# Performance work log

Hardware: AMD Instinct MI355X
Metric: run time of the kernel (lower is better)

Reference implementation:

```python
import jax, jax.numpy as jnp
import numpy as np
from jax import lax

H = 192; W = 192; C = 256; N = H * W; E = 294912; K = 289; DSIG = 1
SLOPE = 0.01
EPS = 1e-5


def leaky(x):
    return jnp.where(x >= 0, x, SLOPE * x)


def conv2d(x, w, pad, groups):
    return lax.conv_general_dilated(
        x, w, (1, 1), [(pad, pad), (pad, pad)],
        dimension_numbers=('NCHW', 'OIHW', 'NCHW'),
        feature_group_count=groups)


def bn2d(x, g, b):
    # BatchNorm2d with track_running_stats=False -> always batch stats (biased var)
    m = x.mean(axis=(0, 2, 3), keepdims=True)
    v = x.var(axis=(0, 2, 3), keepdims=True)
    return (x - m) / jnp.sqrt(v + EPS) * g.reshape(1, -1, 1, 1) + b.reshape(1, -1, 1, 1)


def conv_batch(x, w, g, b, pad, groups):
    # nn.Sequential(LeakyReLU(0.01), Conv2d(bias=False), BatchNorm2d)
    return bn2d(conv2d(leaky(x), w, pad, groups), g, b)


def bn1d(x, g, b):
    m = x.mean(axis=0)
    v = x.var(axis=0)
    return (x - m) / jnp.sqrt(v + EPS) * g + b


def setup_inputs() -> dict:
    key = jax.random.key(0)
    ks = jax.random.split(key, 20)
    X = jax.random.normal(ks[0], (N, C), dtype=jnp.float32)
    src = jax.random.randint(ks[1], (E,), 0, N)
    dst = jax.random.randint(ks[2], (E,), 0, N)
    k1 = jax.random.randint(ks[3], (E,), 0, K)
    k2 = jax.random.randint(ks[4], (E,), 0, K)
    InfoIdx = jnp.stack([src, k1, dst, k2], axis=1).astype(jnp.int64)
    edgmsk = (jax.random.uniform(ks[5], (E, 1)) < 0.9).astype(jnp.float32)
    s = 0.05
    inp = {
        'X': X, 'InfoIdx': InfoIdx, 'edgmsk': edgmsk,
        # PPM: depthwise 17x17 conv_batch then 1x1 conv_batch
        'ppm_w0': jax.random.normal(ks[6], (C, 1, 17, 17), jnp.float32) * s,
        'ppm_g0': jnp.ones((C,), jnp.float32), 'ppm_b0': jnp.zeros((C,), jnp.float32),
        'ppm_w1': jax.random.normal(ks[7], (C, C, 1, 1), jnp.float32) * s,
        'ppm_g1': jnp.ones((C,), jnp.float32), 'ppm_b1': jnp.zeros((C,), jnp.float32),
        # FFN_1: two 1x1 conv_batch
        'ffn1_w0': jax.random.normal(ks[8], (C, C, 1, 1), jnp.float32) * s,
        'ffn1_g0': jnp.ones((C,), jnp.float32), 'ffn1_b0': jnp.zeros((C,), jnp.float32),
        'ffn1_w1': jax.random.normal(ks[9], (C, C, 1, 1), jnp.float32) * s,
        'ffn1_g1': jnp.ones((C,), jnp.float32), 'ffn1_b1': jnp.zeros((C,), jnp.float32),
        # Dis: Linear(C,C) -> LeakyReLU -> Linear(C, 289)
        'dis_w1': jax.random.normal(ks[10], (C, C), jnp.float32) * s,
        'dis_b1': jnp.zeros((C,), jnp.float32),
        'dis_w2': jax.random.normal(ks[11], (K * DSIG, C), jnp.float32) * s,
        'dis_b2': jnp.zeros((K * DSIG,), jnp.float32),
        # BatchNorm1d
        'bn_g': jnp.ones((C,), jnp.float32), 'bn_b': jnp.zeros((C,), jnp.float32),
        # FFN_2 = DoubleConv: depthwise-expand 3x3 (groups=C, out=4C) then 1x1
        'ffn2_w0': jax.random.normal(ks[12], (4 * C, 1, 3, 3), jnp.float32) * s,
        'ffn2_g0': jnp.ones((4 * C,), jnp.float32), 'ffn2_b0': jnp.zeros((4 * C,), jnp.float32),
        'ffn2_w1': jax.random.normal(ks[13], (C, 4 * C, 1, 1), jnp.float32) * s,
        'ffn2_g1': jnp.ones((C,), jnp.float32), 'ffn2_b1': jnp.zeros((C,), jnp.float32),
    }
    return inp


def reference(X, InfoIdx, edgmsk,
              ppm_w0, ppm_g0, ppm_b0, ppm_w1, ppm_g1, ppm_b1,
              ffn1_w0, ffn1_g0, ffn1_b0, ffn1_w1, ffn1_g1, ffn1_b1,
              dis_w1, dis_b1, dis_w2, dis_b2, bn_g, bn_b,
              ffn2_w0, ffn2_g0, ffn2_b0, ffn2_w1, ffn2_g1, ffn2_b1):
    src_idx = InfoIdx[:, 0]
    dst_idx = InfoIdx[:, 2]
    # [N,C] -> [1,C,H,W]
    img = X.T.reshape(1, C, H, W)
    # PPM residual
    t = conv_batch(img, ppm_w0, ppm_g0, ppm_b0, pad=8, groups=C)
    t = conv_batch(t, ppm_w1, ppm_g1, ppm_b1, pad=0, groups=1)
    img = img + t
    # FFN_1 residual
    t = conv_batch(img, ffn1_w0, ffn1_g0, ffn1_b0, pad=0, groups=1)
    t = conv_batch(t, ffn1_w1, ffn1_g1, ffn1_b1, pad=0, groups=1)
    img = img + t
    Xn = img.reshape(C, N).T  # [N, C]
    # Dis MLP -> signal [N, 289, d_signal]
    h = leaky(Xn @ dis_w1.T + dis_b1)
    signal = (h @ dis_w2.T + dis_b2).reshape(N, K, DSIG)
    # edge gather + exp/clamp score
    s_src = signal[src_idx, InfoIdx[:, 1]]  # [E, 1]
    s_dst = signal[dst_idx, InfoIdx[:, 3]]  # [E, 1]
    aij = jnp.exp(jnp.clip(s_src + s_dst, -5.0, 5.0)) * edgmsk  # [E, 1]
    # two scatter-sum reductions to dst nodes
    A_sum = jax.ops.segment_sum(aij, dst_idx, num_segments=N)  # [N, 1]
    XA_sum = jax.ops.segment_sum(Xn[src_idx] * aij, dst_idx, num_segments=N)  # [N, C]
    X_trans = XA_sum / (A_sum + 1e-5)
    Xn = Xn + bn1d(X_trans, bn_g, bn_b)
    # FFN_2 = DoubleConv with residual skip
    img = Xn.T.reshape(1, C, H, W)
    t = conv_batch(img, ffn2_w0, ffn2_g0, ffn2_b0, pad=1, groups=C)
    t = conv_batch(t, ffn2_w1, ffn2_g1, ffn2_b1, pad=0, groups=1)
    out = t + img
    return out.reshape(C, N).T  # final bg.ndata['X'], [N, C]
```

## Files before the change

### kernel.cpp

```cpp
#include <hip/hip_runtime.h>
#include <cstddef>

#define HW 192
#define NP 36864
#define CH 256
#define EDGES 294912
#define KSIG 289
#define SLOPE 0.01f
#define BNEPS 1e-5f

typedef unsigned short u16;
typedef __attribute__((ext_vector_type(8))) short bf16x8;
typedef __attribute__((ext_vector_type(4))) float f32x4;

__device__ __forceinline__ float leaky(float x) { return x >= 0.f ? x : SLOPE * x; }
__device__ __forceinline__ u16 f2bf(float x) {
  unsigned u = __float_as_uint(x);
  unsigned r = (u + 0x7fffu + ((u >> 16) & 1u)) >> 16;
  return (u16)r;
}
__device__ __forceinline__ float bf2f(unsigned h) { return __uint_as_float(h << 16); }
__device__ __forceinline__ void bnss(const float* sums, const float* sqs,
                                     const float* g, const float* b, int k,
                                     float& s, float& h) {
  float mean = sums[k] * (1.f / NP);
  float var = sqs[k] * (1.f / NP) - mean * mean;
  s = g[k] * rsqrtf(var + BNEPS);
  h = b[k] - mean * s;
}

__global__ __launch_bounds__(256) void k_transpose(const float* __restrict__ src,
                                                   float* __restrict__ dst, int R, int S) {
  __shared__ float tile[32][33];
  int s0 = blockIdx.x * 32, r0 = blockIdx.y * 32;
  int tx = threadIdx.x & 31, ty = threadIdx.x >> 5;
#pragma unroll
  for (int j = 0; j < 4; j++) {
    int r = r0 + ty + 8 * j;
    tile[ty + 8 * j][tx] = src[(size_t)r * S + s0 + tx];
  }
  __syncthreads();
#pragma unroll
  for (int j = 0; j < 4; j++) {
    int s = s0 + ty + 8 * j;
    dst[(size_t)s * R + r0 + tx] = tile[tx][ty + 8 * j];
  }
}

__global__ __launch_bounds__(256) void k_cvtW(const float* __restrict__ pw1,
                                              const float* __restrict__ f1w0,
                                              const float* __restrict__ f1w1,
                                              const float* __restrict__ dw1,
                                              const float* __restrict__ dw2,
                                              const float* __restrict__ f2w1,
                                              u16* __restrict__ out) {
  int i = blockIdx.x * 256 + threadIdx.x;
  float v;
  if (i < 65536) v = pw1[i];
  else if (i < 131072) v = f1w0[i - 65536];
  else if (i < 196608) v = f1w1[i - 131072];
  else if (i < 262144) v = dw1[i - 196608];
  else if (i < 360448) { int j = i - 262144; v = (j < KSIG * 256) ? dw2[j] : 0.f; }
  else v = f2w1[i - 360448];
  out[i] = f2bf(v);
}

__global__ __launch_bounds__(256) void k_stats_f32(const float* __restrict__ Xr,
                                                   float* __restrict__ sums,
                                                   float* __restrict__ sqs) {
  int row = blockIdx.x;
  int t = threadIdx.x;
  const float4* p = (const float4*)(Xr + (size_t)row * NP);
  float s = 0.f, q = 0.f;
  for (int i = t; i < NP / 4; i += 256) {
    float4 v = p[i];
    s += v.x + v.y + v.z + v.w;
    q += v.x * v.x + v.y * v.y + v.z * v.z + v.w * v.w;
  }
  __shared__ float ss[256], qq[256];
  ss[t] = s; qq[t] = q;
  __syncthreads();
  for (int d = 128; d > 0; d >>= 1) {
    if (t < d) { ss[t] += ss[t + d]; qq[t] += qq[t + d]; }
    __syncthreads();
  }
  if (t == 0) { sums[row] = ss[0]; sqs[row] = qq[0]; }
}

__global__ __launch_bounds__(256) void k_stats_bf(const u16* __restrict__ Xr,
                                                  float* __restrict__ sums,
                                                  float* __restrict__ sqs) {
  int row = blockIdx.x;
  int t = threadIdx.x;
  const uint4* p = (const uint4*)(Xr + (size_t)row * NP);
  float s = 0.f, q = 0.f;
  for (int i = t; i < NP / 8; i += 256) {
    uint4 v = p[i];
    unsigned w[4] = {v.x, v.y, v.z, v.w};
#pragma unroll
    for (int j = 0; j < 4; j++) {
      float a = bf2f(w[j] & 0xffffu), c = bf2f(w[j] >> 16);
      s += a + c; q += a * a + c * c;
    }
  }
  __shared__ float ss[256], qq[256];
  ss[t] = s; qq[t] = q;
  __syncthreads();
  for (int d = 128; d > 0; d >>= 1) {
    if (t < d) { ss[t] += ss[t + d]; qq[t] += qq[t + d]; }
    __syncthreads();
  }
  if (t == 0) { sums[row] = ss[0]; sqs[row] = qq[0]; }
}

__global__ __launch_bounds__(256) void k_cvtT(const float* __restrict__ in,
                                              u16* __restrict__ outT, int M) {
  __shared__ float tile[32][65];
  int n0 = blockIdx.x * 64, k0 = blockIdx.y * 32;
  int t = threadIdx.x;
#pragma unroll
  for (int i = 0; i < 2; i++) {
    int ci = i * 256 + t;
    int k = ci >> 4, cg = (ci & 15) * 4;
    float4 v = *(const float4*)&in[(size_t)(k0 + k) * NP + n0 + cg];
    tile[k][cg] = v.x; tile[k][cg + 1] = v.y; tile[k][cg + 2] = v.z; tile[k][cg + 3] = v.w;
  }
  __syncthreads();
  int n = t >> 2, kg = (t & 3) * 8;
  uint4 o;
  o.x = (unsigned)f2bf(tile[kg + 0][n]) | ((unsigned)f2bf(tile[kg + 1][n]) << 16);
  o.y = (unsigned)f2bf(tile[kg + 2][n]) | ((unsigned)f2bf(tile[kg + 3][n]) << 16);
  o.z = (unsigned)f2bf(tile[kg + 4][n]) | ((unsigned)f2bf(tile[kg + 5][n]) << 16);
  o.w = (unsigned)f2bf(tile[kg + 6][n]) | ((unsigned)f2bf(tile[kg + 7][n]) << 16);
  *(uint4*)&outT[(size_t)(n0 + n) * M + k0 + kg] = o;
}

__global__ __launch_bounds__(256) void k_cvtTs(const float* __restrict__ in,
                                               u16* __restrict__ outT,
                                               const float* __restrict__ sums,
                                               const float* __restrict__ sqs,
                                               const float* __restrict__ g,
                                               const float* __restrict__ b, int M) {
  __shared__ float tile[32][65];
  int n0 = blockIdx.x * 64, k0 = blockIdx.y * 32;
  int t = threadIdx.x;
#pragma unroll
  for (int i = 0; i < 2; i++) {
    int ci = i * 256 + t;
    int k = ci >> 4, cg = (ci & 15) * 4;
    float s, h; bnss(sums, sqs, g, b, k0 + k, s, h);
    float4 v = *(const float4*)&in[(size_t)(k0 + k) * NP + n0 + cg];
    tile[k][cg]     = leaky(fmaf(v.x, s, h));
    tile[k][cg + 1] = leaky(fmaf(v.y, s, h));
    tile[k][cg + 2] = leaky(fmaf(v.z, s, h));
    tile[k][cg + 3] = leaky(fmaf(v.w, s, h));
  }
  __syncthreads();
  int n = t >> 2, kg = (t & 3) * 8;
  uint4 o;
  o.x = (unsigned)f2bf(tile[kg + 0][n]) | ((unsigned)f2bf(tile[kg + 1][n]) << 16);
  o.y = (unsigned)f2bf(tile[kg + 2][n]) | ((unsigned)f2bf(tile[kg + 3][n]) << 16);
  o.z = (unsigned)f2bf(tile[kg + 4][n]) | ((unsigned)f2bf(tile[kg + 5][n]) << 16);
  o.w = (unsigned)f2bf(tile[kg + 6][n]) | ((unsigned)f2bf(tile[kg + 7][n]) << 16);
  *(uint4*)&outT[(size_t)(n0 + n) * M + k0 + kg] = o;
}

__global__ __launch_bounds__(256) void k_cvtT_bf(const u16* __restrict__ in,
                                                 u16* __restrict__ outT,
                                                 const float* __restrict__ sums,
                                                 const float* __restrict__ sqs,
                                                 const float* __restrict__ g,
                                                 const float* __restrict__ b, int M) {
  __shared__ float tile[32][65];
  int n0 = blockIdx.x * 64, k0 = blockIdx.y * 32;
  int t = threadIdx.x;
  int k = t >> 3, cg = (t & 7) * 8;
  float s, h; bnss(sums, sqs, g, b, k0 + k, s, h);
  uint4 v = *(const uint4*)&in[(size_t)(k0 + k) * NP + n0 + cg];
  unsigned w[4] = {v.x, v.y, v.z, v.w};
#pragma unroll
  for (int j = 0; j < 4; j++) {
    tile[k][cg + 2 * j]     = leaky(fmaf(bf2f(w[j] & 0xffffu), s, h));
    tile[k][cg + 2 * j + 1] = leaky(fmaf(bf2f(w[j] >> 16), s, h));
  }
  __syncthreads();
  int n = t >> 2, kg = (t & 3) * 8;
  uint4 o;
  o.x = (unsigned)f2bf(tile[kg + 0][n]) | ((unsigned)f2bf(tile[kg + 1][n]) << 16);
  o.y = (unsigned)f2bf(tile[kg + 2][n]) | ((unsigned)f2bf(tile[kg + 3][n]) << 16);
  o.z = (unsigned)f2bf(tile[kg + 4][n]) | ((unsigned)f2bf(tile[kg + 5][n]) << 16);
  o.w = (unsigned)f2bf(tile[kg + 6][n]) | ((unsigned)f2bf(tile[kg + 7][n]) << 16);
  *(uint4*)&outT[(size_t)(n0 + n) * M + k0 + kg] = o;
}

__global__ __launch_bounds__(256) void k_fuse1(const float* __restrict__ base,
                                               const float* __restrict__ raw,
                                               const float* __restrict__ sums,
                                               const float* __restrict__ sqs,
                                               const float* __restrict__ g,
                                               const float* __restrict__ b,
                                               float* __restrict__ img2,
                                               u16* __restrict__ outT) {
  __shared__ float tile[32][65];
  int n0 = blockIdx.x * 64, k0 = blockIdx.y * 32;
  int t = threadIdx.x;
#pragma unroll
  for (int i = 0; i < 2; i++) {
    int ci = i * 256 + t;
    int k = ci >> 4, cg = (ci & 15) * 4;
    float s, h; bnss(sums, sqs, g, b, k0 + k, s, h);
    size_t idx = (size_t)(k0 + k) * NP + n0 + cg;
    float4 bv = *(const float4*)&base[idx];
    float4 rv = *(const float4*)&raw[idx];
    float4 o;
    o.x = bv.x + fmaf(rv.x, s, h); o.y = bv.y + fmaf(rv.y, s, h);
    o.z = bv.z + fmaf(rv.z, s, h); o.w = bv.w + fmaf(rv.w, s, h);
    *(float4*)&img2[idx] = o;
    tile[k][cg]     = leaky(o.x);
    tile[k][cg + 1] = leaky(o.y);
    tile[k][cg + 2] = leaky(o.z);
    tile[k][cg + 3] = leaky(o.w);
  }
  __syncthreads();
  int n = t >> 2, kg = (t & 3) * 8;
  uint4 o;
  o.x = (unsigned)f2bf(tile[kg + 0][n]) | ((unsigned)f2bf(tile[kg + 1][n]) << 16);
  o.y = (unsigned)f2bf(tile[kg + 2][n]) | ((unsigned)f2bf(tile[kg + 3][n]) << 16);
  o.z = (unsigned)f2bf(tile[kg + 4][n]) | ((unsigned)f2bf(tile[kg + 5][n]) << 16);
  o.w = (unsigned)f2bf(tile[kg + 6][n]) | ((unsigned)f2bf(tile[kg + 7][n]) << 16);
  *(uint4*)&outT[(size_t)(n0 + n) * CH + k0 + kg] = o;
}

__global__ __launch_bounds__(256) void k_fuse2(const float* __restrict__ base,
                                               const float* __restrict__ raw,
                                               const float* __restrict__ sums,
                                               const float* __restrict__ sqs,
                                               const float* __restrict__ g,
                                               const float* __restrict__ b,
                                               float* __restrict__ XnT,
                                               u16* __restrict__ outT) {
  __shared__ float tile[32][65];
  int n0 = blockIdx.x * 64, k0 = blockIdx.y * 32;
  int t = threadIdx.x;
#pragma unroll
  for (int i = 0; i < 2; i++) {
    int ci = i * 256 + t;
    int k = ci >> 4, cg = (ci & 15) * 4;
    float s, h; bnss(sums, sqs, g, b, k0 + k, s, h);
    size_t idx = (size_t)(k0 + k) * NP + n0 + cg;
    float4 bv = *(const float4*)&base[idx];
    float4 rv = *(const float4*)&raw[idx];
    tile[k][cg]     = bv.x + fmaf(rv.x, s, h);
    tile[k][cg + 1] = bv.y + fmaf(rv.y, s, h);
    tile[k][cg + 2] = bv.z + fmaf(rv.z, s, h);
    tile[k][cg + 3] = bv.w + fmaf(rv.w, s, h);
  }
  __syncthreads();
  int n = t >> 2, kg = (t & 3) * 8;
  float4 f0 = {tile[kg + 0][n], tile[kg + 1][n], tile[kg + 2][n], tile[kg + 3][n]};
  float4 f1 = {tile[kg + 4][n], tile[kg + 5][n], tile[kg + 6][n], tile[kg + 7][n]};
  *(float4*)&XnT[(size_t)(n0 + n) * CH + k0 + kg] = f0;
  *(float4*)&XnT[(size_t)(n0 + n) * CH + k0 + kg + 4] = f1;
  uint4 o;
  o.x = (unsigned)f2bf(f0.x) | ((unsigned)f2bf(f0.y) << 16);
  o.y = (unsigned)f2bf(f0.z) | ((unsigned)f2bf(f0.w) << 16);
  o.z = (unsigned)f2bf(f1.x) | ((unsigned)f2bf(f1.y) << 16);
  o.w = (unsigned)f2bf(f1.z) | ((unsigned)f2bf(f1.w) << 16);
  *(uint4*)&outT[(size_t)(n0 + n) * CH + k0 + kg] = o;
}

__global__ __launch_bounds__(256) void k_mgemm(const u16* __restrict__ A,
                                               const u16* __restrict__ Bt,
                                               float* __restrict__ Out,
                                               const float* __restrict__ bias,
                                               int K, int Mstore, int actout) {
  __shared__ u16 As[128 * 32];
  __shared__ u16 Bs[128 * 32];
  int t = threadIdx.x;
  int lane = t & 63, wave = t >> 6;
  int wm = (wave >> 1) * 64, wn = (wave & 1) * 64;
  int m0 = blockIdx.y * 128, n0 = blockIdx.x * 128;
  int r = lane & 15, q = lane >> 4;
  f32x4 acc[4][4];
#pragma unroll
  for (int a = 0; a < 4; a++)
#pragma unroll
    for (int b = 0; b < 4; b++) acc[a][b] = (f32x4){0.f, 0.f, 0.f, 0.f};

  for (int k0 = 0; k0 < K; k0 += 32) {
#pragma unroll
    for (int i = 0; i < 2; i++) {
      int cc = t + i * 256;
      int mm = cc >> 2, kq = (cc & 3) * 8;
      uint4 av = *(const uint4*)&A[(size_t)(m0 + mm) * K + k0 + kq];
      uint4 bv = *(const uint4*)&Bt[(size_t)(n0 + mm) * K + k0 + kq];
      *(uint4*)&As[mm * 32 + kq] = av;
      *(uint4*)&Bs[mm * 32 + kq] = bv;
    }
    __syncthreads();
    bf16x8 af[4], bfr[4];
#pragma unroll
    for (int mt = 0; mt < 4; mt++)
      af[mt] = *(const bf16x8*)&As[(wm + mt * 16 + r) * 32 + q * 8];
#pragma unroll
    for (int nt = 0; nt < 4; nt++)
      bfr[nt] = *(const bf16x8*)&Bs[(wn + nt * 16 + r) * 32 + q * 8];
#pragma unroll
    for (int mt = 0; mt < 4; mt++)
#pragma unroll
      for (int nt = 0; nt < 4; nt++)
        acc[mt][nt] = __builtin_amdgcn_mfma_f32_16x16x32_bf16(af[mt], bfr[nt], acc[mt][nt], 0, 0, 0);
    __syncthreads();
  }
#pragma unroll
  for (int mt = 0; mt < 4; mt++) {
    int mrow = m0 + wm + mt * 16 + q * 4;
#pragma unroll
    for (int i = 0; i < 4; i++) {
      int m = mrow + i;
      if (m >= Mstore) continue;
      float bs = bias ? bias[m] : 0.f;
#pragma unroll
      for (int nt = 0; nt < 4; nt++) {
        float v = acc[mt][nt][i] + bs;
        if (actout) v = leaky(v);
        Out[(size_t)m * NP + n0 + wn + nt * 16 + r] = v;
      }
    }
  }
}

__global__ __launch_bounds__(256) void k_dwconv17(const float* __restrict__ in,
                                                  const float* __restrict__ w,
                                                  float* __restrict__ out) {
  int c = blockIdx.y;
  int tile = blockIdx.x;
  int ty0 = (tile / 3) * 64, tx0 = (tile % 3) * 64;
  __shared__ u16 smIn[80 * 88];
  __shared__ u16 smT[17 * 16 * 40];
  const float* inc = in + (size_t)c * NP;
  for (int i = threadIdx.x; i < 80 * 80; i += 256) {
    int r = i / 80, cc = i - r * 80;
    int gy = ty0 + r - 8, gx = tx0 + cc - 8;
    float v = 0.f;
    if (gy >= 0 && gy < HW && gx >= 0 && gx < HW) v = leaky(inc[gy * HW + gx]);
    smIn[r * 88 + cc] = f2bf(v);
  }
  const float* wc = w + c * 289;
  for (int i = threadIdx.x; i < 17 * 16 * 32; i += 256) {
    int ky = i >> 9;
    int rem = i & 511;
    int n = rem >> 5, kk = rem & 31;
    int kx = kk - n;
    float v = (kx >= 0 && kx < 17) ? wc[ky * 17 + kx] : 0.f;
    smT[(ky * 16 + n) * 40 + kk] = f2bf(v);
  }
  __syncthreads();
  int lane = threadIdx.x & 63, wave = threadIdx.x >> 6;
  int wy = wave * 16;
  int r = lane & 15, q = lane >> 4;
  f32x4 acc[4];
#pragma unroll
  for (int xt = 0; xt < 4; xt++) acc[xt] = (f32x4){0.f, 0.f, 0.f, 0.f};
#pragma unroll
  for (int ky = 0; ky < 17; ky++) {
    bf16x8 bfrag = *(const bf16x8*)&smT[(ky * 16 + r) * 40 + q * 8];
    int rowA = wy + r + ky;
#pragma unroll
    for (int xt = 0; xt < 4; xt++) {
      bf16x8 afrag = *(const bf16x8*)&smIn[rowA * 88 + xt * 16 + q * 8];
      acc[xt] = __builtin_amdgcn_mfma_f32_16x16x32_bf16(afrag, bfrag, acc[xt], 0, 0, 0);
    }
  }
  float* oc = out + (size_t)c * NP;
#pragma unroll
  for (int xt = 0; xt < 4; xt++) {
    int x = tx0 + xt * 16 + r;
#pragma unroll
    for (int i = 0; i < 4; i++) {
      int y = ty0 + wy + q * 4 + i;
      oc[y * HW + x] = acc[xt][i];
    }
  }
}

__global__ __launch_bounds__(256) void k_conv3x4(const float* __restrict__ in,
                                                 const float* __restrict__ w,
                                                 u16* __restrict__ out) {
  int wave = threadIdx.x >> 6, lane = threadIdx.x & 63;
  int c = blockIdx.y;
  int y = blockIdx.x * 4 + wave;
  const float* wc = w + (size_t)(4 * c) * 9;
  float wr[36];
#pragma unroll
  for (int k = 0; k < 36; k++) wr[k] = wc[k];
  float acc[4][3];
#pragma unroll
  for (int oc = 0; oc < 4; oc++)
#pragma unroll
    for (int s = 0; s < 3; s++) acc[oc][s] = 0.f;
  const float* base = in + (size_t)c * NP;
#pragma unroll
  for (int ky = 0; ky < 3; ky++) {
    int ry = y + ky - 1;
    if (ry < 0 || ry >= HW) continue;
    const float* rp = base + ry * HW;
    float a0 = leaky(rp[lane]);
    float a1 = leaky(rp[64 + lane]);
    float a2 = leaky(rp[128 + lane]);
    float e0 = __shfl(a0, 63), e1 = __shfl(a1, 63);
    float b1 = __shfl(a1, 0),  b2 = __shfl(a2, 0);
    float l0 = __shfl_up(a0, 1); if (lane == 0) l0 = 0.f;
    float l1 = __shfl_up(a1, 1); if (lane == 0) l1 = e0;
    float l2 = __shfl_up(a2, 1); if (lane == 0) l2 = e1;
    float r0 = __shfl_down(a0, 1); if (lane == 63) r0 = b1;
    float r1 = __shfl_down(a1, 1); if (lane == 63) r1 = b2;
    float r2 = __shfl_down(a2, 1); if (lane == 63) r2 = 0.f;
#pragma unroll
    for (int oc = 0; oc < 4; oc++) {
      float w0 = wr[oc * 9 + ky * 3], w1 = wr[oc * 9 + ky * 3 + 1], w2 = wr[oc * 9 + ky * 3 + 2];
      acc[oc][0] = fmaf(w0, l0, fmaf(w1, a0, fmaf(w2, r0, acc[oc][0])));
      acc[oc][1] = fmaf(w0, l1, fmaf(w1, a1, fmaf(w2, r1, acc[oc][1])));
      acc[oc][2] = fmaf(w0, l2, fmaf(w1, a2, fmaf(w2, r2, acc[oc][2])));
    }
  }
  size_t ob = (size_t)(4 * c) * NP + (size_t)y * HW + lane;
#pragma unroll
  for (int oc = 0; oc < 4; oc++) {
    out[ob + (size_t)oc * NP]       = f2bf(acc[oc][0]);
    out[ob + (size_t)oc * NP + 64]  = f2bf(acc[oc][1]);
    out[ob + (size_t)oc * NP + 128] = f2bf(acc[oc][2]);
  }
}

__global__ __launch_bounds__(256) void k_edge(const int* __restrict__ info,
                                              const float* __restrict__ msk,
                                              const float* __restrict__ sig,
                                              float* __restrict__ aij,
                                              int* __restrict__ counts) {
  int e = blockIdx.x * 256 + threadIdx.x;
  int4 ii = ((const int4*)info)[e];
  float s = sig[(size_t)ii.y * NP + ii.x] + sig[(size_t)ii.w * NP + ii.z];
  s = fminf(fmaxf(s, -5.f), 5.f);
  aij[e] = expf(s) * msk[e];
  atomicAdd(&counts[ii.z], 1);
}

__global__ __launch_bounds__(256) void k_scan1(const int* __restrict__ counts,
                                               int* __restrict__ offsets,
                                               int* __restrict__ bsum) {
  __shared__ int sm[256];
  int t = threadIdx.x;
  int i = blockIdx.x * 256 + t;
  int v = counts[i];
  sm[t] = v;
  __syncthreads();
  for (int d = 1; d < 256; d <<= 1) {
    int add = (t >= d) ? sm[t - d] : 0;
    __syncthreads();
    sm[t] += add;
    __syncthreads();
  }
  offsets[i] = sm[t] - v;
  if (t == 255) bsum[blockIdx.x] = sm[255];
}
__global__ __launch_bounds__(256) void k_scan2(const int* __restrict__ bsum,
                                               int* __restrict__ boff) {
  __shared__ int sm[256];
  int t = threadIdx.x;
  int v = (t < 144) ? bsum[t] : 0;
  sm[t] = v;
  __syncthreads();
  for (int d = 1; d < 256; d <<= 1) {
    int add = (t >= d) ? sm[t - d] : 0;
    __syncthreads();
    sm[t] += add;
    __syncthreads();
  }
  boff[t] = sm[t] - v;
}
__global__ __launch_bounds__(256) void k_scan3(int* __restrict__ offsets,
                                               const int* __restrict__ boff,
                                               int* __restrict__ cursor) {
  int i = blockIdx.x * 256 + threadIdx.x;
  int o = offsets[i] + boff[blockIdx.x];
  offsets[i] = o;
  cursor[i] = o;
  if (i == 0) offsets[NP] = EDGES;
}
__global__ __launch_bounds__(256) void k_scatter(const int* __restrict__ info,
                                                 int* __restrict__ cursor,
                                                 int* __restrict__ sorted) {
  int e = blockIdx.x * 256 + threadIdx.x;
  int d = info[4 * e + 2];
  int pos = atomicAdd(&cursor[d], 1);
  sorted[pos] = e;
}

__global__ __launch_bounds__(256) void k_agg(const int* __restrict__ offsets,
                                             const int* __restrict__ sorted,
                                             const float* __restrict__ aij,
                                             const int* __restrict__ info,
                                             const u16* __restrict__ XnBf,
                                             float* __restrict__ Xtr) {
  int wave = threadIdx.x >> 6, lane = threadIdx.x & 63;
  int node = blockIdx.x * 4 + wave;
  int o0 = offsets[node], o1 = offsets[node + 1];
  float ax = 0.f, ay = 0.f, az = 0.f, aw = 0.f, asum = 0.f;
  for (int i = o0; i < o1; i++) {
    int e = sorted[i];
    float a = aij[e];
    int s = info[4 * e];
    uint2 v = ((const uint2*)(XnBf + (size_t)s * CH))[lane];
    ax = fmaf(a, bf2f(v.x & 0xffffu), ax);
    ay = fmaf(a, bf2f(v.x >> 16), ay);
    az = fmaf(a, bf2f(v.y & 0xffffu), az);
    aw = fmaf(a, bf2f(v.y >> 16), aw);
    asum += a;
  }
  float inv = 1.f / (asum + 1e-5f);
  float4 o = {ax * inv, ay * inv, az * inv, aw * inv};
  ((float4*)(Xtr + (size_t)node * CH))[lane] = o;
}

__global__ __launch_bounds__(256) void k_colstats(const float* __restrict__ Xt,
                                                  float* __restrict__ sums,
                                                  float* __restrict__ sqs) {
  int c = threadIdx.x;
  float s = 0.f, q = 0.f;
  for (int n = blockIdx.x; n < NP; n += gridDim.x) {
    float v = Xt[(size_t)n * CH + c];
    s += v; q += v * v;
  }
  atomicAdd(&sums[c], s);
  atomicAdd(&sqs[c], q);
}

__global__ __launch_bounds__(256) void k_mkimg4(const float* __restrict__ Xn,
                                                const float* __restrict__ Xtr,
                                                const float* __restrict__ sums,
                                                const float* __restrict__ sqs,
                                                const float* __restrict__ g,
                                                const float* __restrict__ b,
                                                float* __restrict__ img4) {
  __shared__ float tile[32][33];
  int c0 = blockIdx.x * 32, n0 = blockIdx.y * 32;
  int tx = threadIdx.x & 31, ty = threadIdx.x >> 5;
  int c = c0 + tx;
  float s, h; bnss(sums, sqs, g, b, c, s, h);
#pragma unroll
  for (int j = 0; j < 4; j++) {
    size_t idx = (size_t)(n0 + ty + 8 * j) * CH + c;
    tile[ty + 8 * j][tx] = Xn[idx] + fmaf(Xtr[idx], s, h);
  }
  __syncthreads();
#pragma unroll
  for (int j = 0; j < 4; j++) {
    int cc = c0 + ty + 8 * j;
    img4[(size_t)cc * NP + n0 + tx] = tile[tx][ty + 8 * j];
  }
}

__global__ __launch_bounds__(256) void k_final(const float* __restrict__ raw5,
                                               const float* __restrict__ img4,
                                               const float* __restrict__ sums,
                                               const float* __restrict__ sqs,
                                               const float* __restrict__ g,
                                               const float* __restrict__ b,
                                               float* __restrict__ out) {
  __shared__ float tile[32][33];
  int n0 = blockIdx.x * 32, c0 = blockIdx.y * 32;
  int tx = threadIdx.x & 31, ty = threadIdx.x >> 5;
#pragma unroll
  for (int j = 0; j < 4; j++) {
    int c = c0 + ty + 8 * j;
    float s, h; bnss(sums, sqs, g, b, c, s, h);
    size_t idx = (size_t)c * NP + n0 + tx;
    tile[ty + 8 * j][tx] = fmaf(raw5[idx], s, h) + img4[idx];
  }
  __syncthreads();
#pragma unroll
  for (int j = 0; j < 4; j++) {
    int n = n0 + ty + 8 * j;
    out[(size_t)n * CH + c0 + tx] = tile[tx][ty + 8 * j];
  }
}

extern "C" void kernel_launch(void* const* d_in, const int* in_sizes, int n_in,
                              void* d_out, int out_size, void* d_ws, size_t ws_size,
                              hipStream_t stream) {
  (void)in_sizes; (void)n_in; (void)out_size; (void)ws_size;
  const float* X    = (const float*)d_in[0];
  const int*   info = (const int*)d_in[1];
  const float* msk  = (const float*)d_in[2];
  const float* pw0  = (const float*)d_in[3];
  const float* pg0  = (const float*)d_in[4];
  const float* pb0  = (const float*)d_in[5];
  const float* pw1  = (const float*)d_in[6];
  const float* pg1  = (const float*)d_in[7];
  const float* pb1  = (const float*)d_in[8];
  const float* f1w0 = (const float*)d_in[9];
  const float* f1g0 = (const float*)d_in[10];
  const float* f1b0 = (const float*)d_in[11];
  const float* f1w1 = (const float*)d_in[12];
  const float* f1g1 = (const float*)d_in[13];
  const float* f1b1 = (const float*)d_in[14];
  const float* dw1  = (const float*)d_in[15];
  const float* db1  = (const float*)d_in[16];
  const float* dw2  = (const float*)d_in[17];
  const float* db2  = (const float*)d_in[18];
  const float* bng  = (const float*)d_in[19];
  const float* bnb  = (const float*)d_in[20];
  const float* f2w0 = (const float*)d_in[21];
  const float* f2g0 = (const float*)d_in[22];
  const float* f2b0 = (const float*)d_in[23];
  const float* f2w1 = (const float*)d_in[24];
  const float* f2g1 = (const float*)d_in[25];
  const float* f2b1 = (const float*)d_in[26];
  float* out = (float*)d_out;

  float* ws = (float*)d_ws;
  float* sum0 = ws + 0;    float* sq0 = ws + 256;
  float* sum1 = ws + 512;  float* sq1 = ws + 768;
  float* sum2 = ws + 1024; float* sq2 = ws + 1280;
  float* sum3 = ws + 1536; float* sq3 = ws + 1792;
  float* sum5 = ws + 2048; float* sq5 = ws + 2304;
  float* sumT = ws + 2560; float* sqT = ws + 2816;
  float* sum4 = ws + 3072; float* sq4 = ws + 4096;
  int* counts  = (int*)(ws + 8192);
  int* offsets = (int*)(ws + 45056);
  int* cursor  = (int*)(ws + 82176);
  int* bsum    = (int*)(ws + 119296);
  int* boff    = (int*)(ws + 119552);
  int* sorted  = (int*)(ws + 131072);
  float* aij   = ws + 425984;
  const size_t S = (size_t)NP * CH;
  float* slotD = ws + 720896;
  float* slotB = slotD + S;
  float* slotA = slotB + S;
  float* slotC = slotA + S;
  u16* bfB  = (u16*)(slotC + S);
  u16* bfH  = bfB + S;
  float* sigT = (float*)(bfH + S);
  u16* bfW  = (u16*)(sigT + (size_t)KSIG * NP);
  u16* raw4bf  = (u16*)slotB;
  u16* bfT1024 = bfB;

  hipMemsetAsync(ws, 0, 5120 * sizeof(float), stream);
  hipMemsetAsync(counts, 0, NP * sizeof(int), stream);

  dim3 b256(256);
  k_cvtW<<<2432, b256, 0, stream>>>(pw1, f1w0, f1w1, dw1, dw2, f2w1, bfW);
  k_transpose<<<dim3(CH / 32, NP / 32), b256, 0, stream>>>(X, slotA, NP, CH);
  k_dwconv17<<<dim3(9, CH), b256, 0, stream>>>(slotA, pw0, slotB);
  k_stats_f32<<<CH, b256, 0, stream>>>(slotB, sum0, sq0);
  k_cvtTs<<<dim3(NP / 64, 8), b256, 0, stream>>>(slotB, bfB, sum0, sq0, pg0, pb0, CH);
  k_mgemm<<<dim3(NP / 128, 2), b256, 0, stream>>>(bfW, bfB, slotC, nullptr, CH, CH, 0);
  k_stats_f32<<<CH, b256, 0, stream>>>(slotC, sum1, sq1);
  k_fuse1<<<dim3(NP / 64, 8), b256, 0, stream>>>(slotA, slotC, sum1, sq1, pg1, pb1, slotD, bfB);
  k_mgemm<<<dim3(NP / 128, 2), b256, 0, stream>>>(bfW + 65536, bfB, slotB, nullptr, CH, CH, 0);
  k_stats_f32<<<CH, b256, 0, stream>>>(slotB, sum2, sq2);
  k_cvtTs<<<dim3(NP / 64, 8), b256, 0, stream>>>(slotB, bfB, sum2, sq2, f1g0, f1b0, CH);
  k_mgemm<<<dim3(NP / 128, 2), b256, 0, stream>>>(bfW + 131072, bfB, slotC, nullptr, CH, CH, 0);
  k_stats_f32<<<CH, b256, 0, stream>>>(slotC, sum3, sq3);
  k_fuse2<<<dim3(NP / 64, 8), b256, 0, stream>>>(slotD, slotC, sum3, sq3, f1g1, f1b1, slotA, bfB);
  k_mgemm<<<dim3(NP / 128, 2), b256, 0, stream>>>(bfW + 196608, bfB, slotC, db1, CH, CH, 1);
  k_cvtT<<<dim3(NP / 64, 8), b256, 0, stream>>>(slotC, bfH, CH);
  k_mgemm<<<dim3(NP / 128, 3), b256, 0, stream>>>(bfW + 262144, bfH, sigT, db2, CH, KSIG, 0);
  k_edge<<<EDGES / 256, b256, 0, stream>>>(info, msk, sigT, aij, counts);
  k_scan1<<<NP / 256, b256, 0, stream>>>(counts, offsets, bsum);
  k_scan2<<<1, b256, 0, stream>>>(bsum, boff);
  k_scan3<<<NP / 256, b256, 0, stream>>>(offsets, boff, cursor);
  k_scatter<<<EDGES / 256, b256, 0, stream>>>(info, cursor, sorted);
  k_agg<<<NP / 4, b256, 0, stream>>>(offsets, sorted, aij, info, bfB, slotD);
  k_colstats<<<288, b256, 0, stream>>>(slotD, sumT, sqT);
  k_mkimg4<<<dim3(CH / 32, NP / 32), b256, 0, stream>>>(slotA, slotD, sumT, sqT, bng, bnb, slotC);
  k_conv3x4<<<dim3(48, CH), b256, 0, stream>>>(slotC, f2w0, raw4bf);
  k_stats_bf<<<1024, b256, 0, stream>>>(raw4bf, sum4, sq4);
  k_cvtT_bf<<<dim3(NP / 64, 32), b256, 0, stream>>>(raw4bf, bfT1024, sum4, sq4, f2g0, f2b0, 1024);
  k_mgemm<<<dim3(NP / 128, 2), b256, 0, stream>>>(bfW + 360448, bfT1024, slotD, nullptr, 1024, CH, 0);
  k_stats_f32<<<CH, b256, 0, stream>>>(slotD, sum5, sq5);
  k_final<<<dim3(NP / 32, CH / 32), b256, 0, stream>>>(slotD, slotC, sum5, sq5, f2g1, f2b1, out);
}
```

Baseline: 710.6 us.

## Store intermediate conv/GEMM outputs in bf16 and prepad dwconv input

Raw pre-BatchNorm outputs of the depthwise conv and the 1x1 GEMMs are now written as bf16 instead of fp32. The stats, transpose and fuse kernels read bf16, which roughly halves traffic on these intermediates. The input transpose also writes a zero-padded, leaky-applied bf16 image, and the Toeplitz weight tile is precomputed once per channel, so the 17x17 depthwise conv just does vector copies into shared memory. The cost is an extra memset of the padded buffer, and BN statistics are computed from bf16-rounded values, which adds numerical error.

```diff
diff --git a/kernel.cpp b/kernel.cpp
--- a/kernel.cpp
+++ b/kernel.cpp
@@ -8,6 +8,8 @@
 #define KSIG 289
 #define SLOPE 0.01f
 #define BNEPS 1e-5f
+#define PADW 208
+#define PADSZ (PADW * PADW)
 
 typedef unsigned short u16;
 typedef __attribute__((ext_vector_type(8))) short bf16x8;
@@ -29,21 +31,37 @@
   h = b[k] - mean * s;
 }
 
-__global__ __launch_bounds__(256) void k_transpose(const float* __restrict__ src,
-                                                   float* __restrict__ dst, int R, int S) {
+__global__ __launch_bounds__(256) void k_transpose_pad(const float* __restrict__ src,
+                                                       float* __restrict__ dst,
+                                                       u16* __restrict__ pad) {
   __shared__ float tile[32][33];
   int s0 = blockIdx.x * 32, r0 = blockIdx.y * 32;
   int tx = threadIdx.x & 31, ty = threadIdx.x >> 5;
 #pragma unroll
+  for (int j = 0; j < 4; j++)
+    tile[ty + 8 * j][tx] = src[(size_t)(r0 + ty + 8 * j) * CH + s0 + tx];
+  __syncthreads();
+  int n = r0 + tx;
+  int y = n / HW, x = n - y * HW;
+#pragma unroll
   for (int j = 0; j < 4; j++) {
-    int r = r0 + ty + 8 * j;
-    tile[ty + 8 * j][tx] = src[(size_t)r * S + s0 + tx];
-  }
-  __syncthreads();
-#pragma unroll
-  for (int j = 0; j < 4; j++) {
-    int s = s0 + ty + 8 * j;
-    dst[(size_t)s * R + r0 + tx] = tile[tx][ty + 8 * j];
+    int c = s0 + ty + 8 * j;
+    float v = tile[tx][ty + 8 * j];
+    dst[(size_t)c * NP + n] = v;
+    pad[(size_t)c * PADSZ + (y + 8) * PADW + x + 8] = f2bf(leaky(v));
+  }
+}
+
+__global__ __launch_bounds__(256) void k_mkT(const float* __restrict__ w,
+                                             u16* __restrict__ Tg) {
+  int c = blockIdx.x;
+  const float* wc = w + c * 289;
+  u16* tc = Tg + (size_t)c * 8704;
+  for (int i = threadIdx.x; i < 8704; i += 256) {
+    int ky = i >> 9, rem = i & 511, n = rem >> 5, k = rem & 31;
+    int kx = k - n;
+    float v = (kx >= 0 && kx < 17) ? wc[ky * 17 + kx] : 0.f;
+    tc[i] = f2bf(v);
   }
 }
 
@@ -65,28 +83,6 @@
   out[i] = f2bf(v);
 }
 
-__global__ __launch_bounds__(256) void k_stats_f32(const float* __restrict__ Xr,
-                                                   float* __restrict__ sums,
-                                                   float* __restrict__ sqs) {
-  int row = blockIdx.x;
-  int t = threadIdx.x;
-  const float4* p = (const float4*)(Xr + (size_t)row * NP);
-  float s = 0.f, q = 0.f;
-  for (int i = t; i < NP / 4; i += 256) {
-    float4 v = p[i];
-    s += v.x + v.y + v.z + v.w;
-    q += v.x * v.x + v.y * v.y + v.z * v.z + v.w * v.w;
-  }
-  __shared__ float ss[256], qq[256];
-  ss[t] = s; qq[t] = q;
-  __syncthreads();
-  for (int d = 128; d > 0; d >>= 1) {
-    if (t < d) { ss[t] += ss[t + d]; qq[t] += qq[t + d]; }
-    __syncthreads();
-  }
-  if (t == 0) { sums[row] = ss[0]; sqs[row] = qq[0]; }
-}
-
 __global__ __launch_bounds__(256) void k_stats_bf(const u16* __restrict__ Xr,
                                                   float* __restrict__ sums,
                                                   float* __restrict__ sqs) {
@@ -124,36 +120,6 @@
     int k = ci >> 4, cg = (ci & 15) * 4;
     float4 v = *(const float4*)&in[(size_t)(k0 + k) * NP + n0 + cg];
     tile[k][cg] = v.x; tile[k][cg + 1] = v.y; tile[k][cg + 2] = v.z; tile[k][cg + 3] = v.w;
-  }
-  __syncthreads();
-  int n = t >> 2, kg = (t & 3) * 8;
-  uint4 o;
-  o.x = (unsigned)f2bf(tile[kg + 0][n]) | ((unsigned)f2bf(tile[kg + 1][n]) << 16);
-  o.y = (unsigned)f2bf(tile[kg + 2][n]) | ((unsigned)f2bf(tile[kg + 3][n]) << 16);
-  o.z = (unsigned)f2bf(tile[kg + 4][n]) | ((unsigned)f2bf(tile[kg + 5][n]) << 16);
-  o.w = (unsigned)f2bf(tile[kg + 6][n]) | ((unsigned)f2bf(tile[kg + 7][n]) << 16);
-  *(uint4*)&outT[(size_t)(n0 + n) * M + k0 + kg] = o;
-}
-
-__global__ __launch_bounds__(256) void k_cvtTs(const float* __restrict__ in,
-                                               u16* __restrict__ outT,
-                                               const float* __restrict__ sums,
-                                               const float* __restrict__ sqs,
-                                               const float* __restrict__ g,
-                                               const float* __restrict__ b, int M) {
-  __shared__ float tile[32][65];
-  int n0 = blockIdx.x * 64, k0 = blockIdx.y * 32;
-  int t = threadIdx.x;
-#pragma unroll
-  for (int i = 0; i < 2; i++) {
-    int ci = i * 256 + t;
-    int k = ci >> 4, cg = (ci & 15) * 4;
-    float s, h; bnss(sums, sqs, g, b, k0 + k, s, h);
-    float4 v = *(const float4*)&in[(size_t)(k0 + k) * NP + n0 + cg];
-    tile[k][cg]     = leaky(fmaf(v.x, s, h));
-    tile[k][cg + 1] = leaky(fmaf(v.y, s, h));
-    tile[k][cg + 2] = leaky(fmaf(v.z, s, h));
-    tile[k][cg + 3] = leaky(fmaf(v.w, s, h));
   }
   __syncthreads();
   int n = t >> 2, kg = (t & 3) * 8;
@@ -194,7 +160,7 @@
 }
 
 __global__ __launch_bounds__(256) void k_fuse1(const float* __restrict__ base,
-                                               const float* __restrict__ raw,
+                                               const u16* __restrict__ raw,
                                                const float* __restrict__ sums,
                                                const float* __restrict__ sqs,
                                                const float* __restrict__ g,
@@ -211,10 +177,12 @@
     float s, h; bnss(sums, sqs, g, b, k0 + k, s, h);
     size_t idx = (size_t)(k0 + k) * NP + n0 + cg;
     float4 bv = *(const float4*)&base[idx];
-    float4 rv = *(const float4*)&raw[idx];
+    uint2 rv = *(const uint2*)&raw[idx];
+    float r0 = bf2f(rv.x & 0xffffu), r1 = bf2f(rv.x >> 16);
+    float r2 = bf2f(rv.y & 0xffffu), r3 = bf2f(rv.y >> 16);
     float4 o;
-    o.x = bv.x + fmaf(rv.x, s, h); o.y = bv.y + fmaf(rv.y, s, h);
-    o.z = bv.z + fmaf(rv.z, s, h); o.w = bv.w + fmaf(rv.w, s, h);
+    o.x = bv.x + fmaf(r0, s, h); o.y = bv.y + fmaf(r1, s, h);
+    o.z = bv.z + fmaf(r2, s, h); o.w = bv.w + fmaf(r3, s, h);
     *(float4*)&img2[idx] = o;
     tile[k][cg]     = leaky(o.x);
     tile[k][cg + 1] = leaky(o.y);
@@ -232,7 +200,7 @@
 }
 
 __global__ __launch_bounds__(256) void k_fuse2(const float* __restrict__ base,
-                                               const float* __restrict__ raw,
+                                               const u16* __restrict__ raw,
                                                const float* __restrict__ sums,
                                                const float* __restrict__ sqs,
                                                const float* __restrict__ g,
@@ -249,11 +217,13 @@
     float s, h; bnss(sums, sqs, g, b, k0 + k, s, h);
     size_t idx = (size_t)(k0 + k) * NP + n0 + cg;
     float4 bv = *(const float4*)&base[idx];
-    float4 rv = *(const float4*)&raw[idx];
-    tile[k][cg]     = bv.x + fmaf(rv.x, s, h);
-    tile[k][cg + 1] = bv.y + fmaf(rv.y, s, h);
-    tile[k][cg + 2] = bv.z + fmaf(rv.z, s, h);
-    tile[k][cg + 3] = bv.w + fmaf(rv.w, s, h);
+    uint2 rv = *(const uint2*)&raw[idx];
+    float r0 = bf2f(rv.x & 0xffffu), r1 = bf2f(rv.x >> 16);
+    float r2 = bf2f(rv.y & 0xffffu), r3 = bf2f(rv.y >> 16);
+    tile[k][cg]     = bv.x + fmaf(r0, s, h);
+    tile[k][cg + 1] = bv.y + fmaf(r1, s, h);
+    tile[k][cg + 2] = bv.z + fmaf(r2, s, h);
+    tile[k][cg + 3] = bv.w + fmaf(r3, s, h);
   }
   __syncthreads();
   int n = t >> 2, kg = (t & 3) * 8;
@@ -271,7 +241,8 @@
 
 __global__ __launch_bounds__(256) void k_mgemm(const u16* __restrict__ A,
                                                const u16* __restrict__ Bt,
-                                               float* __restrict__ Out,
+                                               float* __restrict__ Outf,
+                                               u16* __restrict__ Outb,
                                                const float* __restrict__ bias,
                                                int K, int Mstore, int actout) {
   __shared__ u16 As[128 * 32];
@@ -324,36 +295,32 @@
       for (int nt = 0; nt < 4; nt++) {
         float v = acc[mt][nt][i] + bs;
         if (actout) v = leaky(v);
-        Out[(size_t)m * NP + n0 + wn + nt * 16 + r] = v;
+        size_t oi = (size_t)m * NP + n0 + wn + nt * 16 + r;
+        if (Outb) Outb[oi] = f2bf(v); else Outf[oi] = v;
       }
     }
   }
 }
 
-__global__ __launch_bounds__(256) void k_dwconv17(const float* __restrict__ in,
-                                                  const float* __restrict__ w,
-                                                  float* __restrict__ out) {
+__global__ __launch_bounds__(256) void k_dwconv17(const u16* __restrict__ pad,
+                                                  const u16* __restrict__ Tg,
+                                                  u16* __restrict__ outb) {
   int c = blockIdx.y;
   int tile = blockIdx.x;
   int ty0 = (tile / 3) * 64, tx0 = (tile % 3) * 64;
   __shared__ u16 smIn[80 * 88];
   __shared__ u16 smT[17 * 16 * 40];
-  const float* inc = in + (size_t)c * NP;
-  for (int i = threadIdx.x; i < 80 * 80; i += 256) {
-    int r = i / 80, cc = i - r * 80;
-    int gy = ty0 + r - 8, gx = tx0 + cc - 8;
-    float v = 0.f;
-    if (gy >= 0 && gy < HW && gx >= 0 && gx < HW) v = leaky(inc[gy * HW + gx]);
-    smIn[r * 88 + cc] = f2bf(v);
-  }
-  const float* wc = w + c * 289;
-  for (int i = threadIdx.x; i < 17 * 16 * 32; i += 256) {
-    int ky = i >> 9;
-    int rem = i & 511;
-    int n = rem >> 5, kk = rem & 31;
-    int kx = kk - n;
-    float v = (kx >= 0 && kx < 17) ? wc[ky * 17 + kx] : 0.f;
-    smT[(ky * 16 + n) * 40 + kk] = f2bf(v);
+  const u16* pc = pad + (size_t)c * PADSZ;
+  for (int cc = threadIdx.x; cc < 800; cc += 256) {
+    int rr = cc / 10, j = cc - rr * 10;
+    uint4 v = *(const uint4*)(pc + (ty0 + rr) * PADW + tx0 + j * 8);
+    *(uint4*)(smIn + rr * 88 + j * 8) = v;
+  }
+  const u16* tc = Tg + (size_t)c * 8704;
+  for (int cc = threadIdx.x; cc < 1088; cc += 256) {
+    int rr = cc >> 2, j = cc & 3;
+    uint4 v = *(const uint4*)(tc + rr * 32 + j * 8);
+    *(uint4*)(smT + rr * 40 + j * 8) = v;
   }
   __syncthreads();
   int lane = threadIdx.x & 63, wave = threadIdx.x >> 6;
@@ -372,14 +339,14 @@
       acc[xt] = __builtin_amdgcn_mfma_f32_16x16x32_bf16(afrag, bfrag, acc[xt], 0, 0, 0);
     }
   }
-  float* oc = out + (size_t)c * NP;
+  u16* oc = outb + (size_t)c * NP;
 #pragma unroll
   for (int xt = 0; xt < 4; xt++) {
     int x = tx0 + xt * 16 + r;
 #pragma unroll
     for (int i = 0; i < 4; i++) {
       int y = ty0 + wy + q * 4 + i;
-      oc[y * HW + x] = acc[xt][i];
+      oc[y * HW + x] = f2bf(acc[xt][i]);
     }
   }
 }
@@ -561,7 +528,7 @@
   }
 }
 
-__global__ __launch_bounds__(256) void k_final(const float* __restrict__ raw5,
+__global__ __launch_bounds__(256) void k_final(const u16* __restrict__ raw5,
                                                const float* __restrict__ img4,
                                                const float* __restrict__ sums,
                                                const float* __restrict__ sqs,
@@ -576,7 +543,7 @@
     int c = c0 + ty + 8 * j;
     float s, h; bnss(sums, sqs, g, b, c, s, h);
     size_t idx = (size_t)c * NP + n0 + tx;
-    tile[ty + 8 * j][tx] = fmaf(raw5[idx], s, h) + img4[idx];
+    tile[ty + 8 * j][tx] = fmaf(bf2f(raw5[idx]), s, h) + img4[idx];
   }
   __syncthreads();
 #pragma unroll
@@ -643,30 +610,35 @@
   u16* bfH  = bfB + S;
   float* sigT = (float*)(bfH + S);
   u16* bfW  = (u16*)(sigT + (size_t)KSIG * NP);
+  u16* Ppad = (u16*)slotC;
+  u16* Tg   = (u16*)slotD;
   u16* raw4bf  = (u16*)slotB;
   u16* bfT1024 = bfB;
+  u16* raw5bf  = (u16*)slotD;
 
   hipMemsetAsync(ws, 0, 5120 * sizeof(float), stream);
   hipMemsetAsync(counts, 0, NP * sizeof(int), stream);
+  hipMemsetAsync(Ppad, 0, (size_t)PADSZ * CH * sizeof(u16), stream);
 
   dim3 b256(256);
   k_cvtW<<<2432, b256, 0, stream>>>(pw1, f1w0, f1w1, dw1, dw2, f2w1, bfW);
-  k_transpose<<<dim3(CH / 32, NP / 32), b256, 0, stream>>>(X, slotA, NP, CH);
-  k_dwconv17<<<dim3(9, CH), b256, 0, stream>>>(slotA, pw0, slotB);
-  k_stats_f32<<<CH, b256, 0, stream>>>(slotB, sum0, sq0);
-  k_cvtTs<<<dim3(NP / 64, 8), b256, 0, stream>>>(slotB, bfB, sum0, sq0, pg0, pb0, CH);
-  k_mgemm<<<dim3(NP / 128, 2), b256, 0, stream>>>(bfW, bfB, slotC, nullptr, CH, CH, 0);
-  k_stats_f32<<<CH, b256, 0, stream>>>(slotC, sum1, sq1);
-  k_fuse1<<<dim3(NP / 64, 8), b256, 0, stream>>>(slotA, slotC, sum1, sq1, pg1, pb1, slotD, bfB);
-  k_mgemm<<<dim3(NP / 128, 2), b256, 0, stream>>>(bfW + 65536, bfB, slotB, nullptr, CH, CH, 0);
-  k_stats_f32<<<CH, b256, 0, stream>>>(slotB, sum2, sq2);
-  k_cvtTs<<<dim3(NP / 64, 8), b256, 0, stream>>>(slotB, bfB, sum2, sq2, f1g0, f1b0, CH);
-  k_mgemm<<<dim3(NP / 128, 2), b256, 0, stream>>>(bfW + 131072, bfB, slotC, nullptr, CH, CH, 0);
-  k_stats_f32<<<CH, b256, 0, stream>>>(slotC, sum3, sq3);
-  k_fuse2<<<dim3(NP / 64, 8), b256, 0, stream>>>(slotD, slotC, sum3, sq3, f1g1, f1b1, slotA, bfB);
-  k_mgemm<<<dim3(NP / 128, 2), b256, 0, stream>>>(bfW + 196608, bfB, slotC, db1, CH, CH, 1);
+  k_mkT<<<CH, b256, 0, stream>>>(pw0, Tg);
+  k_transpose_pad<<<dim3(CH / 32, NP / 32), b256, 0, stream>>>(X, slotA, Ppad);
+  k_dwconv17<<<dim3(9, CH), b256, 0, stream>>>(Ppad, Tg, bfH);
+  k_stats_bf<<<CH, b256, 0, stream>>>(bfH, sum0, sq0);
+  k_cvtT_bf<<<dim3(NP / 64, 8), b256, 0, stream>>>(bfH, bfB, sum0, sq0, pg0, pb0, CH);
+  k_mgemm<<<dim3(NP / 128, 2), b256, 0, stream>>>(bfW, bfB, nullptr, bfH, nullptr, CH, CH, 0);
+  k_stats_bf<<<CH, b256, 0, stream>>>(bfH, sum1, sq1);
+  k_fuse1<<<dim3(NP / 64, 8), b256, 0, stream>>>(slotA, bfH, sum1, sq1, pg1, pb1, slotD, bfB);
+  k_mgemm<<<dim3(NP / 128, 2), b256, 0, stream>>>(bfW + 65536, bfB, nullptr, bfH, nullptr, CH, CH, 0);
+  k_stats_bf<<<CH, b256, 0, stream>>>(bfH, sum2, sq2);
+  k_cvtT_bf<<<dim3(NP / 64, 8), b256, 0, stream>>>(bfH, bfB, sum2, sq2, f1g0, f1b0, CH);
+  k_mgemm<<<dim3(NP / 128, 2), b256, 0, stream>>>(bfW + 131072, bfB, nullptr, bfH, nullptr, CH, CH, 0);
+  k_stats_bf<<<CH, b256, 0, stream>>>(bfH, sum3, sq3);
+  k_fuse2<<<dim3(NP / 64, 8), b256, 0, stream>>>(slotD, bfH, sum3, sq3, f1g1, f1b1, slotA, bfB);
+  k_mgemm<<<dim3(NP / 128, 2), b256, 0, stream>>>(bfW + 196608, bfB, slotC, nullptr, db1, CH, CH, 1);
   k_cvtT<<<dim3(NP / 64, 8), b256, 0, stream>>>(slotC, bfH, CH);
-  k_mgemm<<<dim3(NP / 128, 3), b256, 0, stream>>>(bfW + 262144, bfH, sigT, db2, CH, KSIG, 0);
+  k_mgemm<<<dim3(NP / 128, 3), b256, 0, stream>>>(bfW + 262144, bfH, sigT, nullptr, db2, CH, KSIG, 0);
   k_edge<<<EDGES / 256, b256, 0, stream>>>(info, msk, sigT, aij, counts);
   k_scan1<<<NP / 256, b256, 0, stream>>>(counts, offsets, bsum);
   k_scan2<<<1, b256, 0, stream>>>(bsum, boff);
@@ -678,7 +650,7 @@
   k_conv3x4<<<dim3(48, CH), b256, 0, stream>>>(slotC, f2w0, raw4bf);
   k_stats_bf<<<1024, b256, 0, stream>>>(raw4bf, sum4, sq4);
   k_cvtT_bf<<<dim3(NP / 64, 32), b256, 0, stream>>>(raw4bf, bfT1024, sum4, sq4, f2g0, f2b0, 1024);
-  k_mgemm<<<dim3(NP / 128, 2), b256, 0, stream>>>(bfW + 360448, bfT1024, slotD, nullptr, 1024, CH, 0);
-  k_stats_f32<<<CH, b256, 0, stream>>>(slotD, sum5, sq5);
-  k_final<<<dim3(NP / 32, CH / 32), b256, 0, stream>>>(slotD, slotC, sum5, sq5, f2g1, f2b1, out);
-}
+  k_mgemm<<<dim3(NP / 128, 2), b256, 0, stream>>>(bfW + 360448, bfT1024, nullptr, raw5bf, nullptr, 1024, CH, 0);
+  k_stats_bf<<<CH, b256, 0, stream>>>(raw5bf, sum5, sq5);
+  k_final<<<dim3(NP / 32, CH / 32), b256, 0, stream>>>(raw5bf, slotC, sum5, sq5, f2g1, f2b1, out);
+}
```

After: 676.6 us. -4.8%, faster.
